# Optimization experiments

Measured on AMD Instinct MI355X. Metric: run time of the kernel, lower is better.

## Reference

```python
import jax, jax.numpy as jnp
import numpy as np

H = 1024          # hidden size
V = 32000         # vocab size
L = 64            # MAX_LENGTH (decode steps, attn width, encoder seq len)
NC = 2            # number of retrieve candidates (encoders = NC + 1)
SOS = 0
EOS = 1


def _gru_step(h, x, W_ih, W_hh, b_ih, b_hh):
    # torch.nn.GRU cell math, gates packed [r, z, n]
    gi = W_ih @ x + b_ih          # [3H]
    gh = W_hh @ h + b_hh          # [3H]
    r = jax.nn.sigmoid(gi[:H] + gh[:H])
    z = jax.nn.sigmoid(gi[H:2 * H] + gh[H:2 * H])
    n = jnp.tanh(gi[2 * H:] + r * gh[2 * H:])
    return (1.0 - z) * n + z * h


def _encode(ids, emb, W_ih, W_hh, b_ih, b_hh):
    # embedding + GRU over the sequence, returns per-step outputs [L, H]
    x = emb[ids]
    def step(h, xt):
        h2 = _gru_step(h, xt, W_ih, W_hh, b_ih, b_hh)
        return h2, h2
    _, outs = jax.lax.scan(step, jnp.zeros((H,), x.dtype), x)
    return outs


def setup_inputs() -> dict:
    key = jax.random.key(0)
    ks = jax.random.split(key, 12)
    s = 0.02
    E = NC + 1
    return {
        "question_ids": jax.random.randint(ks[0], (L,), 0, V),
        "cand_ids": jax.random.randint(ks[1], (NC, L), 0, V),
        # stacked per-encoder params (encoders[0] = question, encoders[1:] = candidates)
        "enc_emb": jax.random.normal(ks[2], (E, V, H), jnp.float32) * s,
        "enc_W_ih": jax.random.normal(ks[3], (E, 3 * H, H), jnp.float32) * s,
        "enc_W_hh": jax.random.normal(ks[4], (E, 3 * H, H), jnp.float32) * s,
        "enc_b_ih": jnp.zeros((E, 3 * H), jnp.float32),
        "enc_b_hh": jnp.zeros((E, 3 * H), jnp.float32),
        # attention decoder params
        "dec_emb": jax.random.normal(ks[5], (V, H), jnp.float32) * s,
        "W_attn": jax.random.normal(ks[6], (L, 2 * H), jnp.float32) * s,
        "b_attn": jnp.zeros((L,), jnp.float32),
        "W_comb": jax.random.normal(ks[7], (H, 2 * H), jnp.float32) * s,
        "b_comb": jnp.zeros((H,), jnp.float32),
        "dec_W_ih": jax.random.normal(ks[8], (3 * H, H), jnp.float32) * s,
        "dec_W_hh": jax.random.normal(ks[9], (3 * H, H), jnp.float32) * s,
        "dec_b_ih": jnp.zeros((3 * H,), jnp.float32),
        "dec_b_hh": jnp.zeros((3 * H,), jnp.float32),
        "W_out": jax.random.normal(ks[10], (V, H), jnp.float32) * s,
        "b_out": jnp.zeros((V,), jnp.float32),
    }


def reference(question_ids, cand_ids, enc_emb, enc_W_ih, enc_W_hh, enc_b_ih,
              enc_b_hh, dec_emb, W_attn, b_attn, W_comb, b_comb, dec_W_ih,
              dec_W_hh, dec_b_ih, dec_b_hh, W_out, b_out):
    # --- multi-encoder ensemble: enc0(question) + (1/n) * sum_i enc_{i+1}(cand_i) ---
    all_ids = jnp.concatenate([question_ids[None, :], cand_ids], axis=0)  # [E, L]
    outs = jax.vmap(_encode)(all_ids, enc_emb, enc_W_ih, enc_W_hh,
                             enc_b_ih, enc_b_hh)                          # [E, L, H]
    enc_outs = outs[0] + outs[1:].sum(axis=0) / NC                        # [L, H]

    # --- greedy attention decode; decoder_hidden starts at initHidden() == zeros ---
    def dec_step(carry, _):
        h, tok, done = carry
        e = dec_emb[tok]                                                  # [H]
        aw = jax.nn.softmax(W_attn @ jnp.concatenate([e, h]) + b_attn)    # [L]
        applied = aw @ enc_outs                                           # [H]
        x = jax.nn.relu(W_comb @ jnp.concatenate([e, applied]) + b_comb)  # [H]
        h2 = _gru_step(h, x, dec_W_ih, dec_W_hh, dec_b_ih, dec_b_hh)
        logp = jax.nn.log_softmax(W_out @ h2 + b_out)                     # [V]
        nxt = jnp.argmax(logp).astype(tok.dtype)                          # topk(1)
        new_done = done | (nxt == EOS)                                    # EOS break -> freeze
        h_out = jnp.where(done, h, h2)
        tok_out = jnp.where(done, tok, nxt)
        return (h_out, tok_out, new_done), (logp, aw, tok_out)

    init = (jnp.zeros((H,), enc_outs.dtype),
            jnp.asarray(SOS, jnp.int32),
            jnp.asarray(False))
    _, (logits, attns, toks) = jax.lax.scan(dec_step, init, None, length=L)
    # logits [L, V], attns [L, L] (decoder_attentions), toks [L] (decoded tokens)
    return logits, attns, toks
```

## Files before the change

kernel.cpp:

```cpp
#include <hip/hip_runtime.h>
#include <cmath>


#define GRID  256
#define TPB   256
#define HD    1024
#define VC    32000
#define LS    64
#define EOS_TOK 1

#define CTRL_BYTES 32768
#define F_H      0
#define F_X      2048
#define F_GH     3072
#define F_SCH    6144
#define F_AW     6208
#define F_PARTV  6272
#define F_M      6528
#define F_ENCOUT 72064
#define F_GI     137600
#define F_OUTS   727424
#define F_WAE    924032
#define WS_FLOATS 2972032

struct __align__(64) Ctrl {
  int epoch; int _p0[15];
  int arrive[GRID * 16];
  int tok; int done; int copy; int _p1[13];
  int partIdx[GRID];
};

#define SSC __HIP_MEMORY_SCOPE_SYSTEM
__device__ __forceinline__ int  ld_rlx(const int* p) {
  return __hip_atomic_load(p, __ATOMIC_RELAXED, SSC);
}
__device__ __forceinline__ void st_rlx(int* p, int v) {
  __hip_atomic_store(p, v, __ATOMIC_RELAXED, SSC);
}
__device__ __forceinline__ float ld_f(const float* p) {
  unsigned u = __hip_atomic_load((const unsigned*)p, __ATOMIC_RELAXED, SSC);
  return __builtin_bit_cast(float, u);
}
__device__ __forceinline__ void st_f(float* p, float v) {
  __hip_atomic_store((unsigned*)p, __builtin_bit_cast(unsigned, v), __ATOMIC_RELAXED, SSC);
}
__device__ __forceinline__ float2 ld_f2(const float* p) {
  unsigned long long u =
      __hip_atomic_load((const unsigned long long*)p, __ATOMIC_RELAXED, SSC);
  return __builtin_bit_cast(float2, u);
}
__device__ __forceinline__ void st_f2(float* p, float2 v) {
  __hip_atomic_store((unsigned long long*)p,
                     __builtin_bit_cast(unsigned long long, v),
                     __ATOMIC_RELAXED, SSC);
}

typedef struct { float4 v[4]; } V16;

__device__ __forceinline__ V16 ldv(const float* __restrict__ p, int lane) {
  V16 r;
#pragma unroll
  for (int c = 0; c < 4; ++c)
    r.v[c] = *(const float4*)(p + c * 256 + lane * 4);
  return r;
}

__device__ __forceinline__ float dot16(const V16& a, const V16& b) {
  float s = 0.f;
#pragma unroll
  for (int c = 0; c < 4; ++c) {
    s = fmaf(a.v[c].x, b.v[c].x, s);
    s = fmaf(a.v[c].y, b.v[c].y, s);
    s = fmaf(a.v[c].z, b.v[c].z, s);
    s = fmaf(a.v[c].w, b.v[c].w, s);
  }
  return s;
}

template <int DCTL>
__device__ __forceinline__ float dppadd(float v) {
  int t = __builtin_amdgcn_update_dpp(0, __builtin_bit_cast(int, v), DCTL, 0xF, 0xF, true);
  return v + __builtin_bit_cast(float, t);
}
__device__ __forceinline__ float dpp_sum63(float v) {
  v = dppadd<0x111>(v);
  v = dppadd<0x112>(v);
  v = dppadd<0x114>(v);
  v = dppadd<0x118>(v);
  v = dppadd<0x142>(v);
  v = dppadd<0x143>(v);
  return v;
}
__device__ __forceinline__ float bcast63(float v) {
  return __builtin_bit_cast(float,
      __builtin_amdgcn_readlane(__builtin_bit_cast(int, v), 63));
}

__device__ __forceinline__ float gru_out(float gir, float giz, float gin,
                                         float ghr, float ghz, float ghn, float hp) {
  float r = 1.f / (1.f + expf(-(gir + ghr)));
  float z = 1.f / (1.f + expf(-(giz + ghz)));
  float n = tanhf(gin + r * ghn);
  return (1.f - z) * n + z * hp;
}

__device__ __forceinline__ void bar_worker(Ctrl* c, int t) {
  __syncthreads();
  if (threadIdx.x == 0) {
    __builtin_amdgcn_s_waitcnt(0);
    st_rlx(&c->arrive[blockIdx.x * 16], t);
    while (ld_rlx(&c->epoch) < t) __builtin_amdgcn_s_sleep(4);
  }
  __syncthreads();
}
__device__ __forceinline__ void bar_master_wait(Ctrl* c, int t) {
  __syncthreads();
  if (threadIdx.x > 0) {
    while (ld_rlx(&c->arrive[threadIdx.x * 16]) < t) __builtin_amdgcn_s_sleep(1);
  }
  __syncthreads();
}
__device__ __forceinline__ void bar_master_release(Ctrl* c, int t) {
  __syncthreads();
  if (threadIdx.x == 0) {
    __builtin_amdgcn_s_waitcnt(0);
    st_rlx(&c->epoch, t);
  }
  __syncthreads();
}

__device__ void decode_prepare(int s, Ctrl* c, float* __restrict__ fb,
                               const float* __restrict__ b_attn,
                               float* __restrict__ out_attns,
                               float* __restrict__ out_toks) {
  const int tid = threadIdx.x;
  __shared__ float s_v[TPB];
  __shared__ int   s_i[TPB];
  int frozen = 0;
  if (s > 0) {
    int done_entry = ld_rlx(&c->done);
    if (!done_entry) {
      s_v[tid] = ld_f(fb + F_PARTV + tid);
      s_i[tid] = ld_rlx(&c->partIdx[tid]);
      __syncthreads();
      for (int st = TPB / 2; st > 0; st >>= 1) {
        if (tid < st) {
          float ov = s_v[tid + st]; int oi = s_i[tid + st];
          if (ov > s_v[tid] || (ov == s_v[tid] && oi < s_i[tid])) { s_v[tid] = ov; s_i[tid] = oi; }
        }
        __syncthreads();
      }
      int nxt = s_i[0];
      if (tid == 0) {
        out_toks[s - 1] = (float)nxt;
        st_rlx(&c->tok, nxt);
        if (nxt == EOS_TOK) st_rlx(&c->done, 1);
      }
    } else {
      frozen = 1;
      if (tid == 0) { out_toks[s - 1] = (float)ld_rlx(&c->tok); st_rlx(&c->copy, 1); }
      if (s < LS && tid < LS) out_attns[s * LS + tid] = out_attns[(s - 1) * LS + tid];
    }
  }
  if (s >= LS || frozen) return;
  __syncthreads();
  int tok = ld_rlx(&c->tok);
  if (tid < LS) {
    float sc = fb[F_WAE + (size_t)tok * LS + tid] + ld_f(fb + F_SCH + tid) + b_attn[tid];
    float m = sc;
    for (int off = 32; off > 0; off >>= 1) m = fmaxf(m, __shfl_xor(m, off, 64));
    float ex = expf(sc - m);
    float sum = ex;
    for (int off = 32; off > 0; off >>= 1) sum += __shfl_xor(sum, off, 64);
    float a = ex / sum;
    st_f(fb + F_AW + tid, a);
    out_attns[s * LS + tid] = a;
  }
}

__global__ void __launch_bounds__(TPB, 1)
seq2seq_kernel(const int* __restrict__ qids, const int* __restrict__ cand,
               const float* __restrict__ enc_emb, const float* __restrict__ enc_Wih,
               const float* __restrict__ enc_Whh, const float* __restrict__ enc_bih,
               const float* __restrict__ enc_bhh, const float* __restrict__ dec_emb,
               const float* __restrict__ W_attn, const float* __restrict__ b_attn,
               const float* __restrict__ W_comb, const float* __restrict__ b_comb,
               const float* __restrict__ dWih, const float* __restrict__ dWhh,
               const float* __restrict__ dbih, const float* __restrict__ dbhh,
               const float* __restrict__ Wout, const float* __restrict__ bout,
               float* __restrict__ out, float* __restrict__ ws) {
  Ctrl* c = (Ctrl*)ws;
  float* fb = (float*)((char*)ws + CTRL_BYTES);
  const int tid = threadIdx.x;
  const int wg = blockIdx.x;
  const int wid = tid >> 6;
  const int lane = tid & 63;
  float* out_attns = out + (size_t)LS * VC;
  float* out_toks = out_attns + LS * LS;
  int bt = 0;

  __shared__ float s_h[3][HD];
  __shared__ float s_vec[HD];
  __shared__ float s_lv[4]; __shared__ int s_li[4];

#define GRID_BARRIER() do { ++bt; \
    if (wg == 0) { bar_master_wait(c, bt); bar_master_release(c, bt); } \
    else bar_worker(c, bt); } while (0)

  {
    int gw = wg * 4 + wid;
#pragma unroll 1
    for (int task = gw; task < 2304 + VC; task += GRID * 4) {
      if (task < 2304) {
        int r0 = task * 4;
        int e = r0 / 3072;
        int rL = r0 - e * 3072;
        const float* Wr = enc_Wih + (size_t)e * 3 * HD * HD + (size_t)rL * HD;
        V16 w0 = ldv(Wr, lane), w1 = ldv(Wr + HD, lane);
        V16 w2 = ldv(Wr + 2 * HD, lane), w3 = ldv(Wr + 3 * HD, lane);
        const int* ids = (e == 0) ? qids : (cand + (e - 1) * LS);
        float b0 = enc_bih[e * 3 * HD + rL + 0];
        float b1 = enc_bih[e * 3 * HD + rL + 1];
        float b2 = enc_bih[e * 3 * HD + rL + 2];
        float b3 = enc_bih[e * 3 * HD + rL + 3];
#pragma unroll 1
        for (int t = 0; t < LS; ++t) {
          int tk = ids[t];
          V16 xv = ldv(enc_emb + ((size_t)e * VC + tk) * HD, lane);
          float s0 = dpp_sum63(dot16(w0, xv));
          float s1 = dpp_sum63(dot16(w1, xv));
          float s2 = dpp_sum63(dot16(w2, xv));
          float s3 = dpp_sum63(dot16(w3, xv));
          if (lane == 63) {
            float* dst = fb + F_GI + (size_t)(e * LS + t) * 3 * HD + rL;
            st_f2(dst, make_float2(s0 + b0, s1 + b1));
            st_f2(dst + 2, make_float2(s2 + b2, s3 + b3));
          }
        }
      } else {
        int cc = task - 2304;
        V16 ev = ldv(dec_emb + (size_t)cc * HD, lane);
        float myval = 0.f;
#pragma unroll 1
        for (int k = 0; k < LS; k += 4) {
          float a0 = dot16(ldv(W_attn + (size_t)(k + 0) * 2 * HD, lane), ev);
          float a1 = dot16(ldv(W_attn + (size_t)(k + 1) * 2 * HD, lane), ev);
          float a2 = dot16(ldv(W_attn + (size_t)(k + 2) * 2 * HD, lane), ev);
          float a3 = dot16(ldv(W_attn + (size_t)(k + 3) * 2 * HD, lane), ev);
          a0 = bcast63(dpp_sum63(a0));
          a1 = bcast63(dpp_sum63(a1));
          a2 = bcast63(dpp_sum63(a2));
          a3 = bcast63(dpp_sum63(a3));
          myval = (lane == k + 0) ? a0 : myval;
          myval = (lane == k + 1) ? a1 : myval;
          myval = (lane == k + 2) ? a2 : myval;
          myval = (lane == k + 3) ? a3 : myval;
        }
        st_f(fb + F_WAE + (size_t)cc * LS + lane, myval);
      }
    }
  }
  GRID_BARRIER();

#pragma unroll 1
  for (int t = 0; t < LS; ++t) {
#pragma unroll
    for (int k2 = 0; k2 < 6; ++k2) {
      int off = k2 * 256 + tid;
      int e = off >> 9, rem = off & 511;
      float2 v = make_float2(0.f, 0.f);
      if (t > 0) v = ld_f2(fb + F_OUTS + (size_t)(e * LS + (t - 1)) * HD + rem * 2);
      *(float2*)&s_h[e][rem * 2] = v;
    }
    __syncthreads();
    int j = wg * 4 + wid;
#pragma unroll 1
    for (int e = 0; e < 3; ++e) {
      const float* Whh = enc_Whh + (size_t)e * 3 * HD * HD;
      V16 hv = ldv(&s_h[e][0], lane);
      float ghr = dpp_sum63(dot16(ldv(Whh + (size_t)j * HD, lane), hv));
      float ghz = dpp_sum63(dot16(ldv(Whh + (size_t)(HD + j) * HD, lane), hv));
      float ghn = dpp_sum63(dot16(ldv(Whh + (size_t)(2 * HD + j) * HD, lane), hv));
      if (lane == 63) {
        ghr += enc_bhh[e * 3 * HD + j];
        ghz += enc_bhh[e * 3 * HD + HD + j];
        ghn += enc_bhh[e * 3 * HD + 2 * HD + j];
        const float* gi = fb + F_GI + (size_t)(e * LS + t) * 3 * HD;
        float hp = s_h[e][j];
        st_f(fb + F_OUTS + (size_t)(e * LS + t) * HD + j,
             gru_out(gi[j], gi[HD + j], gi[2 * HD + j], ghr, ghz, ghn, hp));
      }
    }
    GRID_BARRIER();
  }

  {
    int gt = wg * TPB + tid;
    float o0 = fb[F_OUTS + gt];
    float o1 = fb[F_OUTS + 65536 + gt];
    float o2 = fb[F_OUTS + 131072 + gt];
    st_f(fb + F_ENCOUT + gt, o0 + 0.5f * (o1 + o2));
    if (gt < 3 * HD) st_f(fb + F_GH + gt, dbhh[gt]);
    if (gt < LS) st_f(fb + F_SCH + gt, 0.f);
  }
  GRID_BARRIER();

  {
    int r = wg * 4 + wid;
    V16 wr = ldv(W_comb + (size_t)r * 2 * HD + HD, lane);
#pragma unroll 1
    for (int t = 0; t < LS; ++t) {
      float s = dpp_sum63(dot16(wr, ldv(fb + F_ENCOUT + (size_t)t * HD, lane)));
      if (lane == 63) st_f(fb + F_M + r * LS + t, s);
    }
  }
  ++bt;
  if (wg == 0) { bar_master_wait(c, bt); decode_prepare(0, c, fb, b_attn, out_attns, out_toks); bar_master_release(c, bt); }
  else bar_worker(c, bt);

#pragma unroll 1
  for (int s = 0; s < LS; ++s) {
    int cp = ld_rlx(&c->copy);
    const int hcur = F_H + (s & 1) * HD;
    const int hnew = F_H + ((s + 1) & 1) * HD;

    if (!cp) {
      int tok = ld_rlx(&c->tok);
      int r = wg * 4 + wid;
      V16 ev = ldv(dec_emb + (size_t)tok * HD, lane);
      V16 wr = ldv(W_comb + (size_t)r * 2 * HD, lane);
      float p = dot16(wr, ev);
      if (lane < 16) {
        float4 m4 = *(const float4*)(fb + F_M + r * LS + lane * 4);
        float2 a01 = ld_f2(fb + F_AW + lane * 4);
        float2 a23 = ld_f2(fb + F_AW + lane * 4 + 2);
        p = fmaf(m4.x, a01.x, p); p = fmaf(m4.y, a01.y, p);
        p = fmaf(m4.z, a23.x, p); p = fmaf(m4.w, a23.y, p);
      }
      float sum = dpp_sum63(p);
      if (lane == 63) st_f(fb + F_X + r, fmaxf(sum + b_comb[r], 0.f));
    }
    GRID_BARRIER();

    if (!cp) {
#pragma unroll
      for (int k2 = 0; k2 < 2; ++k2) {
        int off = k2 * 256 + tid;
        *(float2*)&s_vec[off * 2] = ld_f2(fb + F_X + off * 2);
      }
      __syncthreads();
      int j = wg * 4 + wid;
      V16 xv = ldv(s_vec, lane);
      float g0 = dpp_sum63(dot16(ldv(dWih + (size_t)j * HD, lane), xv));
      float g1 = dpp_sum63(dot16(ldv(dWih + (size_t)(HD + j) * HD, lane), xv));
      float g2 = dpp_sum63(dot16(ldv(dWih + (size_t)(2 * HD + j) * HD, lane), xv));
      if (lane == 63) {
        g0 += dbih[j]; g1 += dbih[HD + j]; g2 += dbih[2 * HD + j];
        float ghr = ld_f(fb + F_GH + j);
        float ghz = ld_f(fb + F_GH + HD + j);
        float ghn = ld_f(fb + F_GH + 2 * HD + j);
        float hp = ld_f(fb + hcur + j);
        st_f(fb + hnew + j, gru_out(g0, g1, g2, ghr, ghz, ghn, hp));
      }
      __syncthreads();
    }
    GRID_BARRIER();

    if (cp) {
      if (tid < 125) {
        int i = wg * 125 + tid;
        st_f(out + (size_t)s * VC + i, out[(size_t)(s - 1) * VC + i]);
      }
    } else {
#pragma unroll
      for (int k2 = 0; k2 < 2; ++k2) {
        int off = k2 * 256 + tid;
        *(float2*)&s_vec[off * 2] = ld_f2(fb + hnew + off * 2);
      }
      __syncthreads();
      V16 hv = ldv(s_vec, lane);
      for (int q = wid; q < 12; q += 4) {
        int row = wg * 12 + q;
        float g = dpp_sum63(dot16(ldv(dWhh + (size_t)row * HD, lane), hv));
        if (lane == 63) st_f(fb + F_GH + row, g + dbhh[row]);
      }
      if (wg < LS && wid == 0) {
        float g = dpp_sum63(dot16(ldv(W_attn + (size_t)wg * 2 * HD + HD, lane), hv));
        if (lane == 63) st_f(fb + F_SCH + wg, g);
      }
      int base = wg * 125;
      int lo = wid * 32;
      int hi = (lo + 32 < 125) ? lo + 32 : 125;
      float bestv = -3.0e38f; int bestr = 0x7FFFFFFF;
#pragma unroll 1
      for (int rr = lo; rr < hi; rr += 4) {
        int i1 = (rr + 1 < hi) ? rr + 1 : hi - 1;
        int i2 = (rr + 2 < hi) ? rr + 2 : hi - 1;
        int i3 = (rr + 3 < hi) ? rr + 3 : hi - 1;
        int r0 = base + rr, r1 = base + i1, r2 = base + i2, r3 = base + i3;
        V16 w0 = ldv(Wout + (size_t)r0 * HD, lane);
        V16 w1 = ldv(Wout + (size_t)r1 * HD, lane);
        V16 w2 = ldv(Wout + (size_t)r2 * HD, lane);
        V16 w3 = ldv(Wout + (size_t)r3 * HD, lane);
        float p0 = dot16(w0, hv), p1 = dot16(w1, hv);
        float p2 = dot16(w2, hv), p3 = dot16(w3, hv);
        float v0 = bcast63(dpp_sum63(p0)) + bout[r0];
        float v1 = bcast63(dpp_sum63(p1)) + bout[r1];
        float v2 = bcast63(dpp_sum63(p2)) + bout[r2];
        float v3 = bcast63(dpp_sum63(p3)) + bout[r3];
        float sv = (lane == 0) ? v0 : (lane == 1) ? v1 : (lane == 2) ? v2 : v3;
        if (lane < 4 && rr + lane < hi)
          st_f(out + (size_t)s * VC + r0 + lane, sv);
        if (v0 > bestv) { bestv = v0; bestr = r0; }
        if (v1 > bestv) { bestv = v1; bestr = r1; }
        if (v2 > bestv) { bestv = v2; bestr = r2; }
        if (v3 > bestv) { bestv = v3; bestr = r3; }
      }
      if (lane == 0) { s_lv[wid] = bestv; s_li[wid] = bestr; }
      __syncthreads();
      if (tid == 0) {
        float bv = s_lv[0]; int bi = s_li[0];
#pragma unroll
        for (int q2 = 1; q2 < 4; ++q2)
          if (s_lv[q2] > bv || (s_lv[q2] == bv && s_li[q2] < bi)) { bv = s_lv[q2]; bi = s_li[q2]; }
        st_f(fb + F_PARTV + wg, bv);
        st_rlx(&c->partIdx[wg], bi);
      }
    }
    ++bt;
    if (wg == 0) { bar_master_wait(c, bt); decode_prepare(s + 1, c, fb, b_attn, out_attns, out_toks); bar_master_release(c, bt); }
    else bar_worker(c, bt);
  }

  if (wg < LS) {
    __shared__ float s_red[TPB];
    float* row = out + (size_t)wg * VC;
    float m = -3.0e38f;
    for (int i = tid; i < VC; i += TPB) m = fmaxf(m, row[i]);
    s_red[tid] = m; __syncthreads();
    for (int st = TPB / 2; st > 0; st >>= 1) {
      if (tid < st) s_red[tid] = fmaxf(s_red[tid], s_red[tid + st]);
      __syncthreads();
    }
    float rowmax = s_red[0]; __syncthreads();
    float sum = 0.f;
    for (int i = tid; i < VC; i += TPB) sum += expf(row[i] - rowmax);
    s_red[tid] = sum; __syncthreads();
    for (int st = TPB / 2; st > 0; st >>= 1) {
      if (tid < st) s_red[tid] += s_red[tid + st];
      __syncthreads();
    }
    float lse = rowmax + logf(s_red[0]);
    __syncthreads();
    for (int i = tid; i < VC; i += TPB) row[i] -= lse;
  }
}

extern "C" void kernel_launch(void* const* d_in, const int* in_sizes, int n_in,
                              void* d_out, int out_size, void* d_ws, size_t ws_size,
                              hipStream_t stream) {
  (void)in_sizes; (void)n_in; (void)out_size; (void)ws_size;
  hipMemsetAsync(d_ws, 0, CTRL_BYTES + 2 * HD * sizeof(float), stream);

  const int* qids = (const int*)d_in[0];
  const int* cand = (const int*)d_in[1];
  const float* enc_emb = (const float*)d_in[2];
  const float* enc_Wih = (const float*)d_in[3];
  const float* enc_Whh = (const float*)d_in[4];
  const float* enc_bih = (const float*)d_in[5];
  const float* enc_bhh = (const float*)d_in[6];
  const float* dec_emb = (const float*)d_in[7];
  const float* W_attn = (const float*)d_in[8];
  const float* b_attn = (const float*)d_in[9];
  const float* W_comb = (const float*)d_in[10];
  const float* b_comb = (const float*)d_in[11];
  const float* dWih = (const float*)d_in[12];
  const float* dWhh = (const float*)d_in[13];
  const float* dbih = (const float*)d_in[14];
  const float* dbhh = (const float*)d_in[15];
  const float* Wout = (const float*)d_in[16];
  const float* bout = (const float*)d_in[17];
  float* outp = (float*)d_out;
  float* wsp = (float*)d_ws;

  void* args[] = { &qids, &cand, &enc_emb, &enc_Wih, &enc_Whh, &enc_bih, &enc_bhh,
                   &dec_emb, &W_attn, &b_attn, &W_comb, &b_comb, &dWih, &dWhh,
                   &dbih, &dbhh, &Wout, &bout, &outp, &wsp };
  hipLaunchCooperativeKernel(reinterpret_cast<void*>(seq2seq_kernel),
                             dim3(GRID), dim3(TPB), args, 0, stream);
}
```

Measured before the change: 3.849 ms.

## Use int8 Wout for per-step argmax with exact candidate rescoring and deferred logits

Quantizes W_out to int8 with per-row scales in the prologue and uses it for the per-step greedy argmax. Candidates within a provable error bound (from the quantization residual norm and the hidden-state norm) are rescored exactly in fp32 by workgroup 0. The exact fp32 logits for all steps are computed after the decode loop from stored hidden states, with W_out rows held in registers and reused across the 64 steps. This cuts per-step W_out traffic by about 4x on the serial critical path. In exchange it adds prologue quantization work, a candidate-rescoring phase on a single workgroup, and an extra barrier.

Result: slower. 4.570 ms (+18.7%).

```diff
diff --git a/kernel.cpp b/kernel.cpp
--- a/kernel.cpp
+++ b/kernel.cpp
@@ -21,12 +21,16 @@
 #define F_GI     137600
 #define F_OUTS   727424
 #define F_WAE    924032
-#define WS_FLOATS 2972032
+#define F_HALL   2972032
+#define F_QSC    3037568
+#define F_CAND   3069568
+#define F_WQ     3086336
+#define CAND_CAP 8192
 
 struct __align__(64) Ctrl {
   int epoch; int _p0[15];
   int arrive[GRID * 16];
-  int tok; int done; int copy; int _p1[13];
+  int tok; int done; int copy; int candN; int rnmax; int _p1[11];
   int partIdx[GRID];
 };
 
@@ -54,6 +58,9 @@
                      __builtin_bit_cast(unsigned long long, v),
                      __ATOMIC_RELAXED, SSC);
 }
+__device__ __forceinline__ void st_u64(void* p, unsigned long long v) {
+  __hip_atomic_store((unsigned long long*)p, v, __ATOMIC_RELAXED, SSC);
+}
 
 typedef struct { float4 v[4]; } V16;
 
@@ -62,6 +69,17 @@
 #pragma unroll
   for (int c = 0; c < 4; ++c)
     r.v[c] = *(const float4*)(p + c * 256 + lane * 4);
+  return r;
+}
+
+__device__ __forceinline__ V16 ldv_u(const float* p, int lane) {
+  V16 r;
+#pragma unroll
+  for (int c = 0; c < 4; ++c) {
+    float2 a = ld_f2(p + c * 256 + lane * 4);
+    float2 b = ld_f2(p + c * 256 + lane * 4 + 2);
+    r.v[c] = make_float4(a.x, a.y, b.x, b.y);
+  }
   return r;
 }
 
@@ -74,6 +92,22 @@
     s = fmaf(a.v[c].z, b.v[c].z, s);
     s = fmaf(a.v[c].w, b.v[c].w, s);
   }
+  return s;
+}
+
+__device__ __forceinline__ float idot4(unsigned u, float4 h, float s) {
+  s = fmaf((float)(int)(signed char)(u & 255u), h.x, s);
+  s = fmaf((float)(int)(signed char)((u >> 8) & 255u), h.y, s);
+  s = fmaf((float)(int)(signed char)((u >> 16) & 255u), h.z, s);
+  s = fmaf((float)(int)(signed char)(u >> 24), h.w, s);
+  return s;
+}
+__device__ __forceinline__ float idot16(const uint4 q, const V16& h) {
+  float s = 0.f;
+  s = idot4(q.x, h.v[0], s);
+  s = idot4(q.y, h.v[1], s);
+  s = idot4(q.z, h.v[2], s);
+  s = idot4(q.w, h.v[3], s);
   return s;
 }
 
@@ -91,9 +125,36 @@
   v = dppadd<0x143>(v);
   return v;
 }
+template <int DCTL>
+__device__ __forceinline__ float dppmax_(float v) {
+  int t = __builtin_amdgcn_update_dpp(0, __builtin_bit_cast(int, v), DCTL, 0xF, 0xF, true);
+  return fmaxf(v, __builtin_bit_cast(float, t));
+}
+__device__ __forceinline__ float dpp_max63(float v) {
+  v = dppmax_<0x111>(v);
+  v = dppmax_<0x112>(v);
+  v = dppmax_<0x114>(v);
+  v = dppmax_<0x118>(v);
+  v = dppmax_<0x142>(v);
+  v = dppmax_<0x143>(v);
+  return v;
+}
 __device__ __forceinline__ float bcast63(float v) {
   return __builtin_bit_cast(float,
       __builtin_amdgcn_readlane(__builtin_bit_cast(int, v), 63));
+}
+
+__device__ __forceinline__ float sumsq4(float4 a) {
+  return fmaf(a.x, a.x, fmaf(a.y, a.y, fmaf(a.z, a.z, a.w * a.w)));
+}
+__device__ __forceinline__ float block_sum256(float v, float* s_red, int tid) {
+  s_red[tid] = v; __syncthreads();
+  for (int st = TPB / 2; st > 0; st >>= 1) {
+    if (tid < st) s_red[tid] += s_red[tid + st];
+    __syncthreads();
+  }
+  float r = s_red[0]; __syncthreads();
+  return r;
 }
 
 __device__ __forceinline__ float gru_out(float gir, float giz, float gin,
@@ -131,35 +192,84 @@
 
 __device__ void decode_prepare(int s, Ctrl* c, float* __restrict__ fb,
                                const float* __restrict__ b_attn,
+                               const float* __restrict__ Wout,
+                               const float* __restrict__ bout,
                                float* __restrict__ out_attns,
                                float* __restrict__ out_toks) {
   const int tid = threadIdx.x;
   __shared__ float s_v[TPB];
-  __shared__ int   s_i[TPB];
+  __shared__ int   s_ci[1024];
+  __shared__ float s_cv[1024];
+  __shared__ int   s_cn;
   int frozen = 0;
   if (s > 0) {
     int done_entry = ld_rlx(&c->done);
     if (!done_entry) {
-      s_v[tid] = ld_f(fb + F_PARTV + tid);
-      s_i[tid] = ld_rlx(&c->partIdx[tid]);
-      __syncthreads();
+      float pv = ld_f(fb + F_PARTV + tid);
+      s_v[tid] = pv; __syncthreads();
       for (int st = TPB / 2; st > 0; st >>= 1) {
-        if (tid < st) {
-          float ov = s_v[tid + st]; int oi = s_i[tid + st];
-          if (ov > s_v[tid] || (ov == s_v[tid] && oi < s_i[tid])) { s_v[tid] = ov; s_i[tid] = oi; }
+        if (tid < st) s_v[tid] = fmaxf(s_v[tid], s_v[tid + st]);
+        __syncthreads();
+      }
+      float gmax = s_v[0];
+      const float* hb = fb + F_H + (s & 1) * HD;
+      float2 ha = ld_f2(hb + tid * 4);
+      float2 hc = ld_f2(hb + tid * 4 + 2);
+      float4 h4 = make_float4(ha.x, ha.y, hc.x, hc.y);
+      __syncthreads();
+      float ssq = block_sum256(sumsq4(h4), s_v, tid);
+      float hn = sqrtf(ssq) * 1.00001f;
+      float rmx = __int_as_float(ld_rlx(&c->rnmax));
+      float Wp = fmaf(2.0f * rmx, hn, 4e-6f * (1.0f + hn));
+      float T = gmax - Wp;
+      if (tid == 0) s_cn = 0;
+      __syncthreads();
+      if (pv >= T) {
+        int k = atomicAdd(&s_cn, 1);
+        if (k < 1024) s_ci[k] = ld_rlx(&c->partIdx[tid]);
+      }
+      int nap = ld_rlx(&c->candN); if (nap > CAND_CAP) nap = CAND_CAP;
+      for (int k2 = tid; k2 < nap; k2 += TPB) {
+        float av = ld_f(fb + F_CAND + 2 * k2);
+        if (av >= T) {
+          int k = atomicAdd(&s_cn, 1);
+          if (k < 1024) s_ci[k] = ld_rlx((int*)(fb + F_CAND) + 2 * k2 + 1);
         }
-        __syncthreads();
-      }
-      int nxt = s_i[0];
+      }
+      __syncthreads();
+      int m = s_cn; if (m > 1024) m = 1024;
+      {
+        int pw = tid >> 6, pl = tid & 63;
+        V16 hvv = ldv_u(hb, pl);
+        for (int k = pw; k < m; k += 4) {
+          int row = s_ci[k];
+          V16 w = ldv(Wout + (size_t)row * HD, pl);
+          float ex = bcast63(dpp_sum63(dot16(w, hvv))) + bout[row];
+          if (pl == 0) s_cv[k] = ex;
+        }
+      }
+      __syncthreads();
       if (tid == 0) {
-        out_toks[s - 1] = (float)nxt;
-        st_rlx(&c->tok, nxt);
-        if (nxt == EOS_TOK) st_rlx(&c->done, 1);
+        float bv = s_cv[0]; int bi = s_ci[0];
+        for (int k = 1; k < m; ++k)
+          if (s_cv[k] > bv || (s_cv[k] == bv && s_ci[k] < bi)) { bv = s_cv[k]; bi = s_ci[k]; }
+        out_toks[s - 1] = (float)bi;
+        st_rlx(&c->tok, bi);
+        if (bi == EOS_TOK) st_rlx(&c->done, 1);
+        st_rlx(&c->candN, 0);
       }
     } else {
       frozen = 1;
       if (tid == 0) { out_toks[s - 1] = (float)ld_rlx(&c->tok); st_rlx(&c->copy, 1); }
-      if (s < LS && tid < LS) out_attns[s * LS + tid] = out_attns[(s - 1) * LS + tid];
+      if (s < LS) {
+        if (tid < LS) out_attns[s * LS + tid] = out_attns[(s - 1) * LS + tid];
+#pragma unroll
+        for (int k2 = 0; k2 < 4; ++k2) {
+          int i = k2 * 256 + tid;
+          st_f(fb + F_HALL + (size_t)s * HD + i,
+               ld_f(fb + F_HALL + (size_t)(s - 1) * HD + i));
+        }
+      }
     }
   }
   if (s >= LS || frozen) return;
@@ -201,7 +311,11 @@
 
   __shared__ float s_h[3][HD];
   __shared__ float s_vec[HD];
+  __shared__ float s_vecp[HD];
+  __shared__ float s_red[TPB];
+  __shared__ float s_apx[128];
   __shared__ float s_lv[4]; __shared__ int s_li[4];
+  __shared__ float s_bbv; __shared__ int s_bbi;
 
 #define GRID_BARRIER() do { ++bt; \
     if (wg == 0) { bar_master_wait(c, bt); bar_master_release(c, bt); } \
@@ -209,8 +323,9 @@
 
   {
     int gw = wg * 4 + wid;
-#pragma unroll 1
-    for (int task = gw; task < 2304 + VC; task += GRID * 4) {
+    float lrmax = 0.f;
+#pragma unroll 1
+    for (int task = gw; task < 2304 + 2 * VC; task += GRID * 4) {
       if (task < 2304) {
         int r0 = task * 4;
         int e = r0 / 3072;
@@ -237,7 +352,7 @@
             st_f2(dst + 2, make_float2(s2 + b2, s3 + b3));
           }
         }
-      } else {
+      } else if (task < 2304 + VC) {
         int cc = task - 2304;
         V16 ev = ldv(dec_emb + (size_t)cc * HD, lane);
         float myval = 0.f;
@@ -257,8 +372,49 @@
           myval = (lane == k + 3) ? a3 : myval;
         }
         st_f(fb + F_WAE + (size_t)cc * LS + lane, myval);
-      }
-    }
+      } else {
+        int r = task - (2304 + VC);
+        const float* wl = Wout + (size_t)r * HD + lane * 16;
+        float4 a0 = *(const float4*)(wl);
+        float4 a1 = *(const float4*)(wl + 4);
+        float4 a2 = *(const float4*)(wl + 8);
+        float4 a3 = *(const float4*)(wl + 12);
+        float mx = fmaxf(
+            fmaxf(fmaxf(fabsf(a0.x), fabsf(a0.y)), fmaxf(fabsf(a0.z), fabsf(a0.w))),
+            fmaxf(fmaxf(fabsf(a1.x), fabsf(a1.y)), fmaxf(fabsf(a1.z), fabsf(a1.w))));
+        mx = fmaxf(mx, fmaxf(
+            fmaxf(fmaxf(fabsf(a2.x), fabsf(a2.y)), fmaxf(fabsf(a2.z), fabsf(a2.w))),
+            fmaxf(fmaxf(fabsf(a3.x), fabsf(a3.y)), fmaxf(fabsf(a3.z), fabsf(a3.w)))));
+        mx = bcast63(dpp_max63(mx));
+        float scale = fmaxf(mx, 1e-30f) * (1.0f / 127.0f);
+        float inv = 1.0f / scale;
+        float r2 = 0.f;
+        unsigned wq0, wq1, wq2, wq3;
+#pragma unroll
+        for (int cq = 0; cq < 4; ++cq) {
+          float4 aa = (cq == 0) ? a0 : (cq == 1) ? a1 : (cq == 2) ? a2 : a3;
+          int q0 = __float2int_rn(aa.x * inv); q0 = q0 > 127 ? 127 : (q0 < -127 ? -127 : q0);
+          int q1 = __float2int_rn(aa.y * inv); q1 = q1 > 127 ? 127 : (q1 < -127 ? -127 : q1);
+          int q2 = __float2int_rn(aa.z * inv); q2 = q2 > 127 ? 127 : (q2 < -127 ? -127 : q2);
+          int q3 = __float2int_rn(aa.w * inv); q3 = q3 > 127 ? 127 : (q3 < -127 ? -127 : q3);
+          float d;
+          d = fmaf(-scale, (float)q0, aa.x); r2 = fmaf(d, d, r2);
+          d = fmaf(-scale, (float)q1, aa.y); r2 = fmaf(d, d, r2);
+          d = fmaf(-scale, (float)q2, aa.z); r2 = fmaf(d, d, r2);
+          d = fmaf(-scale, (float)q3, aa.w); r2 = fmaf(d, d, r2);
+          unsigned w = (unsigned)(q0 & 255) | ((unsigned)(q1 & 255) << 8) |
+                       ((unsigned)(q2 & 255) << 16) | ((unsigned)(q3 & 255) << 24);
+          if (cq == 0) wq0 = w; else if (cq == 1) wq1 = w; else if (cq == 2) wq2 = w; else wq3 = w;
+        }
+        float r2s = bcast63(dpp_sum63(r2));
+        char* qrow = (char*)(fb + F_WQ) + (size_t)r * 1024 + lane * 16;
+        st_u64(qrow, (unsigned long long)wq0 | ((unsigned long long)wq1 << 32));
+        st_u64(qrow + 8, (unsigned long long)wq2 | ((unsigned long long)wq3 << 32));
+        if (lane == 0) st_f(fb + F_QSC + r, scale);
+        lrmax = fmaxf(lrmax, sqrtf(r2s));
+      }
+    }
+    if (lane == 0) atomicMax(&c->rnmax, __float_as_int(lrmax));
   }
   GRID_BARRIER();
 
@@ -315,7 +471,7 @@
     }
   }
   ++bt;
-  if (wg == 0) { bar_master_wait(c, bt); decode_prepare(0, c, fb, b_attn, out_attns, out_toks); bar_master_release(c, bt); }
+  if (wg == 0) { bar_master_wait(c, bt); decode_prepare(0, c, fb, b_attn, Wout, bout, out_attns, out_toks); bar_master_release(c, bt); }
   else bar_worker(c, bt);
 
 #pragma unroll 1
@@ -360,24 +516,33 @@
         float ghz = ld_f(fb + F_GH + HD + j);
         float ghn = ld_f(fb + F_GH + 2 * HD + j);
         float hp = ld_f(fb + hcur + j);
-        st_f(fb + hnew + j, gru_out(g0, g1, g2, ghr, ghz, ghn, hp));
+        float hval = gru_out(g0, g1, g2, ghr, ghz, ghn, hp);
+        st_f(fb + hnew + j, hval);
+        st_f(fb + F_HALL + (size_t)s * HD + j, hval);
       }
       __syncthreads();
     }
     GRID_BARRIER();
 
-    if (cp) {
-      if (tid < 125) {
-        int i = wg * 125 + tid;
-        st_f(out + (size_t)s * VC + i, out[(size_t)(s - 1) * VC + i]);
-      }
-    } else {
+    if (!cp) {
 #pragma unroll
       for (int k2 = 0; k2 < 2; ++k2) {
         int off = k2 * 256 + tid;
         *(float2*)&s_vec[off * 2] = ld_f2(fb + hnew + off * 2);
       }
-      __syncthreads();
+      {
+        int cI = tid >> 6, lI = tid & 63;
+        float2 pa = ld_f2(fb + hnew + lI * 16 + cI * 4);
+        float2 pb = ld_f2(fb + hnew + lI * 16 + cI * 4 + 2);
+        *(float4*)&s_vecp[cI * 256 + lI * 4] = make_float4(pa.x, pa.y, pb.x, pb.y);
+      }
+      __syncthreads();
+      float4 hh4 = *(const float4*)&s_vec[tid * 4];
+      float ssq = block_sum256(sumsq4(hh4), s_red, tid);
+      float hn = sqrtf(ssq) * 1.00001f;
+      float rmx = __int_as_float(ld_rlx(&c->rnmax));
+      float Wp = fmaf(2.0f * rmx, hn, 4e-6f * (1.0f + hn));
+      float Wwork = Wp * 1.5f + 1e-7f;
       V16 hv = ldv(s_vec, lane);
       for (int q = wid; q < 12; q += 4) {
         int row = wg * 12 + q;
@@ -388,6 +553,8 @@
         float g = dpp_sum63(dot16(ldv(W_attn + (size_t)wg * 2 * HD + HD, lane), hv));
         if (lane == 63) st_f(fb + F_SCH + wg, g);
       }
+      V16 hq = ldv(s_vecp, lane);
+      const unsigned char* qb = (const unsigned char*)(fb + F_WQ);
       int base = wg * 125;
       int lo = wid * 32;
       int hi = (lo + 32 < 125) ? lo + 32 : 125;
@@ -398,19 +565,18 @@
         int i2 = (rr + 2 < hi) ? rr + 2 : hi - 1;
         int i3 = (rr + 3 < hi) ? rr + 3 : hi - 1;
         int r0 = base + rr, r1 = base + i1, r2 = base + i2, r3 = base + i3;
-        V16 w0 = ldv(Wout + (size_t)r0 * HD, lane);
-        V16 w1 = ldv(Wout + (size_t)r1 * HD, lane);
-        V16 w2 = ldv(Wout + (size_t)r2 * HD, lane);
-        V16 w3 = ldv(Wout + (size_t)r3 * HD, lane);
-        float p0 = dot16(w0, hv), p1 = dot16(w1, hv);
-        float p2 = dot16(w2, hv), p3 = dot16(w3, hv);
-        float v0 = bcast63(dpp_sum63(p0)) + bout[r0];
-        float v1 = bcast63(dpp_sum63(p1)) + bout[r1];
-        float v2 = bcast63(dpp_sum63(p2)) + bout[r2];
-        float v3 = bcast63(dpp_sum63(p3)) + bout[r3];
+        uint4 q0 = *(const uint4*)(qb + (size_t)r0 * 1024 + lane * 16);
+        uint4 q1 = *(const uint4*)(qb + (size_t)r1 * 1024 + lane * 16);
+        uint4 q2 = *(const uint4*)(qb + (size_t)r2 * 1024 + lane * 16);
+        uint4 q3 = *(const uint4*)(qb + (size_t)r3 * 1024 + lane * 16);
+        float p0 = idot16(q0, hq), p1 = idot16(q1, hq);
+        float p2 = idot16(q2, hq), p3 = idot16(q3, hq);
+        float v0 = bcast63(dpp_sum63(p0)) * fb[F_QSC + r0] + bout[r0];
+        float v1 = bcast63(dpp_sum63(p1)) * fb[F_QSC + r1] + bout[r1];
+        float v2 = bcast63(dpp_sum63(p2)) * fb[F_QSC + r2] + bout[r2];
+        float v3 = bcast63(dpp_sum63(p3)) * fb[F_QSC + r3] + bout[r3];
         float sv = (lane == 0) ? v0 : (lane == 1) ? v1 : (lane == 2) ? v2 : v3;
-        if (lane < 4 && rr + lane < hi)
-          st_f(out + (size_t)s * VC + r0 + lane, sv);
+        if (lane < 4 && rr + lane < hi) s_apx[rr + lane] = sv;
         if (v0 > bestv) { bestv = v0; bestr = r0; }
         if (v1 > bestv) { bestv = v1; bestr = r1; }
         if (v2 > bestv) { bestv = v2; bestr = r2; }
@@ -423,17 +589,78 @@
 #pragma unroll
         for (int q2 = 1; q2 < 4; ++q2)
           if (s_lv[q2] > bv || (s_lv[q2] == bv && s_li[q2] < bi)) { bv = s_lv[q2]; bi = s_li[q2]; }
+        s_bbv = bv; s_bbi = bi;
         st_f(fb + F_PARTV + wg, bv);
         st_rlx(&c->partIdx[wg], bi);
       }
+      __syncthreads();
+      if (tid < 125) {
+        float a = s_apx[tid];
+        if (base + tid != s_bbi && a >= s_bbv - Wwork) {
+          int n = atomicAdd(&c->candN, 1);
+          if (n < CAND_CAP) {
+            st_f(fb + F_CAND + 2 * n, a);
+            st_rlx((int*)(fb + F_CAND) + 2 * n + 1, base + tid);
+          }
+        }
+      }
     }
     ++bt;
-    if (wg == 0) { bar_master_wait(c, bt); decode_prepare(s + 1, c, fb, b_attn, out_attns, out_toks); bar_master_release(c, bt); }
+    if (wg == 0) { bar_master_wait(c, bt); decode_prepare(s + 1, c, fb, b_attn, Wout, bout, out_attns, out_toks); bar_master_release(c, bt); }
     else bar_worker(c, bt);
   }
 
+  {
+    int base2 = wg * 125;
+#pragma unroll 1
+    for (int gg = wid; gg < 16; gg += 4) {
+      int rr = gg * 8;
+      int e1 = rr + 1 < 125 ? rr + 1 : 124;
+      int e2 = rr + 2 < 125 ? rr + 2 : 124;
+      int e3 = rr + 3 < 125 ? rr + 3 : 124;
+      int e4 = rr + 4 < 125 ? rr + 4 : 124;
+      int e5 = rr + 5 < 125 ? rr + 5 : 124;
+      int e6 = rr + 6 < 125 ? rr + 6 : 124;
+      int e7 = rr + 7 < 125 ? rr + 7 : 124;
+      V16 w0 = ldv(Wout + (size_t)(base2 + rr) * HD, lane);
+      V16 w1 = ldv(Wout + (size_t)(base2 + e1) * HD, lane);
+      V16 w2 = ldv(Wout + (size_t)(base2 + e2) * HD, lane);
+      V16 w3 = ldv(Wout + (size_t)(base2 + e3) * HD, lane);
+      V16 w4 = ldv(Wout + (size_t)(base2 + e4) * HD, lane);
+      V16 w5 = ldv(Wout + (size_t)(base2 + e5) * HD, lane);
+      V16 w6 = ldv(Wout + (size_t)(base2 + e6) * HD, lane);
+      V16 w7 = ldv(Wout + (size_t)(base2 + e7) * HD, lane);
+      float b0 = bout[base2 + rr], b1 = bout[base2 + e1];
+      float b2 = bout[base2 + e2], b3 = bout[base2 + e3];
+      float b4 = bout[base2 + e4], b5 = bout[base2 + e5];
+      float b6 = bout[base2 + e6], b7 = bout[base2 + e7];
+#pragma unroll 1
+      for (int s2 = 0; s2 < LS; ++s2) {
+        V16 hvv = ldv(fb + F_HALL + (size_t)s2 * HD, lane);
+        float v0 = bcast63(dpp_sum63(dot16(w0, hvv))) + b0;
+        float v1 = bcast63(dpp_sum63(dot16(w1, hvv))) + b1;
+        float v2 = bcast63(dpp_sum63(dot16(w2, hvv))) + b2;
+        float v3 = bcast63(dpp_sum63(dot16(w3, hvv))) + b3;
+        float v4 = bcast63(dpp_sum63(dot16(w4, hvv))) + b4;
+        float v5 = bcast63(dpp_sum63(dot16(w5, hvv))) + b5;
+        float v6 = bcast63(dpp_sum63(dot16(w6, hvv))) + b6;
+        float v7 = bcast63(dpp_sum63(dot16(w7, hvv))) + b7;
+        float sv = v0;
+        sv = (lane == 1) ? v1 : sv;
+        sv = (lane == 2) ? v2 : sv;
+        sv = (lane == 3) ? v3 : sv;
+        sv = (lane == 4) ? v4 : sv;
+        sv = (lane == 5) ? v5 : sv;
+        sv = (lane == 6) ? v6 : sv;
+        sv = (lane == 7) ? v7 : sv;
+        if (lane < 8 && rr + lane < 125)
+          st_f(out + (size_t)s2 * VC + base2 + rr + lane, sv);
+      }
+    }
+  }
+  GRID_BARRIER();
+
   if (wg < LS) {
-    __shared__ float s_red[TPB];
     float* row = out + (size_t)wg * VC;
     float m = -3.0e38f;
     for (int i = tid; i < VC; i += TPB) m = fmaxf(m, row[i]);
```
